# Kernel tuning notes

Measured on AMD Instinct MI355X. Metric: run time of the kernel, lower is better.

The kernel has to match this reference:

```python
import jax, jax.numpy as jnp
import numpy as np

N_LEVELS = 16
N_FEATS = 2
TABLE_SIZE = 1 << 19          # log2_hashmap_size = 19
BASE_RES = 32
PER_LEVEL_SCALE = 1.3819
RES = 512
CLAMP = 25.133
PRIME_Y = np.uint32(2654435761)
N_PTS = 1 << 19


def hashgrid_encode(table, uv):
    """Instant-NGP style multires hashgrid. table: [L, T, F], uv: [N, 2] in [0,1].
    Returns [N, L*F]."""
    L, T, F = table.shape
    levels = jnp.arange(L)
    res = jnp.floor(BASE_RES * (PER_LEVEL_SCALE ** levels.astype(jnp.float32))).astype(jnp.int32)  # [L]
    # 4 bilinear corner offsets
    offs = jnp.array([[0, 0], [1, 0], [0, 1], [1, 1]], dtype=jnp.int32)  # [4, 2]

    def level_fn(tab_l, res_l):
        pos = uv * res_l.astype(uv.dtype)                       # [N, 2]
        p0 = jnp.clip(jnp.floor(pos).astype(jnp.int32), 0, res_l - 1)
        frac = pos - p0.astype(uv.dtype)                        # [N, 2]
        corners = p0[:, None, :] + offs[None, :, :]             # [N, 4, 2]
        cx = corners[..., 0].astype(jnp.uint32)
        cy = corners[..., 1].astype(jnp.uint32)
        stride = (res_l + 1).astype(jnp.uint32)
        dense_idx = cx + cy * stride                            # dense grid index
        hash_idx = (cx ^ (cy * PRIME_Y)) & jnp.uint32(T - 1)    # spatial hash (T is pow2)
        use_dense = (res_l + 1).astype(jnp.int64) * (res_l + 1).astype(jnp.int64) <= T
        idx = jnp.where(use_dense, dense_idx, hash_idx).astype(jnp.int32)  # [N, 4]
        feats = tab_l[idx]                                      # [N, 4, F] gather
        wx, wy = frac[:, 0], frac[:, 1]
        w = jnp.stack([(1 - wx) * (1 - wy), wx * (1 - wy),
                       (1 - wx) * wy, wx * wy], axis=-1)        # [N, 4]
        return jnp.einsum('ncf,nc->nf', feats, w)               # [N, F]

    out = jax.vmap(level_fn)(table, res)                        # [L, N, F]
    return out.transpose(1, 0, 2).reshape(uv.shape[0], L * F)


def sin_layer(x, W, b):
    h = jnp.clip(x @ W.T + b, -CLAMP, CLAMP)
    return jnp.sin(h)


def setup_inputs() -> dict:
    key = jax.random.key(0)
    ks = jax.random.split(key, 8)
    y = jax.random.randint(ks[0], (N_PTS,), 0, RES, dtype=jnp.int32)
    x = jax.random.randint(ks[1], (N_PTS,), 0, RES, dtype=jnp.int32)
    cam_feat = jax.random.normal(ks[2], (32,), dtype=jnp.float32)
    # NGP tables initialized uniform in [-1e-4, 1e-4]
    table = jax.random.uniform(ks[3], (N_LEVELS, TABLE_SIZE, N_FEATS),
                               minval=-1e-4, maxval=1e-4, dtype=jnp.float32)
    def siren_w(k, outp, inp):
        return jax.random.uniform(k, (outp, inp), minval=-1.0 / inp, maxval=1.0 / inp,
                                  dtype=jnp.float32)
    W1 = siren_w(ks[4], 512, 64)
    W2 = siren_w(ks[5], 512, 512)
    W3 = siren_w(ks[6], 384, 512)
    return {"y": y, "x": x, "cam_feat": cam_feat, "table": table,
            "W1": W1, "b1": jnp.zeros((512,), jnp.float32),
            "W2": W2, "b2": jnp.zeros((512,), jnp.float32),
            "W3": W3, "b3": jnp.zeros((384,), jnp.float32)}


def reference(y, x, cam_feat, table, W1, b1, W2, b2, W3, b3):
    denom = jnp.float32(RES - 1)
    uv = jnp.stack([jnp.clip(x.astype(jnp.float32), 0, RES - 1) / denom,
                    jnp.clip(y.astype(jnp.float32), 0, RES - 1) / denom], axis=-1)  # [N, 2]
    codes = hashgrid_encode(table, uv)                          # [N, 32]
    cam = jnp.broadcast_to(cam_feat[None, :], (codes.shape[0], cam_feat.shape[0]))
    h = jnp.concatenate([codes, cam], axis=-1)                  # [N, 64]
    h = sin_layer(h, W1, b1)
    h = sin_layer(h, W2, b2)
    return sin_layer(h, W3, b3)                                 # [N, 384]
```

## Files before the change

### kernel.cpp

```cpp
#include <hip/hip_runtime.h>

typedef _Float16 half8 __attribute__((ext_vector_type(8)));
typedef _Float16 half4 __attribute__((ext_vector_type(4)));
typedef _Float16 half2v __attribute__((ext_vector_type(2)));
typedef float f32x4 __attribute__((ext_vector_type(4)));

#define TSIZE (1 << 19)
#define TMASK (TSIZE - 1)

__constant__ int c_res[16] = {32, 44, 61, 84, 116, 161, 222, 307,
                              425, 588, 812, 1123, 1551, 2144, 2963, 4095};

__global__ void hg_cvt_all(const float* __restrict__ W1, const float* __restrict__ W2,
                           const float* __restrict__ W3, _Float16* __restrict__ d) {
  int g = blockIdx.x * blockDim.x + threadIdx.x;
  int i = g * 4;
  const float* s;
  if (i < 32768) s = W1 + i;
  else if (i < 32768 + 262144) s = W2 + (i - 32768);
  else s = W3 + (i - 32768 - 262144);
  float4 v = *(const float4*)s;
  half4 h = {(_Float16)v.x, (_Float16)v.y, (_Float16)v.z, (_Float16)v.w};
  *(half4*)(d + i) = h;
}

__device__ __forceinline__ float sin_act_precise(float x) {
  if (__builtin_expect(fabsf(x) > 1.0f, 0))
    return sinf(fminf(fmaxf(x, -25.133f), 25.133f));
  float x2 = x * x;
  float p = 2.75573192e-6f;
  p = fmaf(p, x2, -1.98412698e-4f);
  p = fmaf(p, x2, 8.33333333e-3f);
  p = fmaf(p, x2, -1.66666667e-1f);
  return fmaf(p * x2, x, x);
}

__device__ __forceinline__ float sin_act_fast(float x) {
  return __sinf(fminf(fmaxf(x, -25.133f), 25.133f));
}

#define XROW 144
#define SBASE 18432
#define SROW 1040
#define LD_X(m, k) (*(const half8*)(&smem[(m) * XROW + (k) * 2]))
#define LD_S(m, k) (*(const half8*)(&smem[SBASE + (m) * SROW + (k) * 2]))
#define ST_S8(m, n, v) \
  do { *(half4*)(&smem[SBASE + (m) * SROW + (n) * 2]) = (v); } while (0)

#define MFMA16 __builtin_amdgcn_mfma_f32_16x16x32_f16

__global__ void __launch_bounds__(1024, 4)
hg_fused(const int* __restrict__ ybuf, const int* __restrict__ xbuf,
         const float* __restrict__ cam, const float* __restrict__ table,
         const _Float16* __restrict__ W1h, const float* __restrict__ b1,
         const _Float16* __restrict__ W2h, const float* __restrict__ b2,
         const _Float16* __restrict__ W3h, const float* __restrict__ b3,
         float* __restrict__ out) {
  __shared__ __align__(16) unsigned char smem[151552];
  const int t = threadIdx.x;
  const int lane = t & 63;
  const int wid = t >> 6;
  const int l15 = lane & 15;
  const int lhi = lane >> 4;
  const int rowh = wid & 1;
  const int colg = wid >> 1;
  const int mrow0 = rowh * 64;
  const int pbase = blockIdx.x << 7;
  const f32x4 vzero = {0.f, 0.f, 0.f, 0.f};

  {
    const int sub = t & 15;
    const int res = c_res[sub];
    const float rf = (float)res;
    const unsigned strd = (unsigned)(res + 1);
    const bool dense = (res <= 723);
    const float* tb = table + ((size_t)sub * TSIZE) * 2;
    const float2 cf = ((const float2*)cam)[sub];
    const half2v hc = {(_Float16)cf.x, (_Float16)cf.y};
#pragma unroll
    for (int hh = 0; hh < 2; ++hh) {
      const int m = (t >> 4) + hh * 64;
      const int p = pbase + m;
      const float u = (float)xbuf[p] / 511.0f;
      const float v = (float)ybuf[p] / 511.0f;
      const float px = u * rf, py = v * rf;
      int p0x = (int)floorf(px); p0x = p0x < 0 ? 0 : (p0x > res - 1 ? res - 1 : p0x);
      int p0y = (int)floorf(py); p0y = p0y < 0 ? 0 : (p0y > res - 1 ? res - 1 : p0y);
      const float fx = px - (float)p0x, fy = py - (float)p0y;
      const float w00 = (1.f - fx) * (1.f - fy), w10 = fx * (1.f - fy);
      const float w01 = (1.f - fx) * fy, w11 = fx * fy;
      float c0 = 0.f, c1 = 0.f;
#pragma unroll
      for (int c = 0; c < 4; ++c) {
        const unsigned cx = (unsigned)(p0x + (c & 1));
        const unsigned cy = (unsigned)(p0y + (c >> 1));
        const unsigned idx = dense ? (cx + cy * strd)
                                   : ((cx ^ (cy * 2654435761u)) & TMASK);
        const float2 f = *(const float2*)(tb + (size_t)idx * 2);
        const float w = (c == 0) ? w00 : (c == 1) ? w10 : (c == 2) ? w01 : w11;
        c0 = fmaf(w, f.x, c0);
        c1 = fmaf(w, f.y, c1);
      }
      half2v hf = {(_Float16)c0, (_Float16)c1};
      *(half2v*)(&smem[m * XROW + 4 * sub]) = hf;
      *(half2v*)(&smem[m * XROW + 64 + 4 * sub]) = hc;
    }
  }
  __syncthreads();

  {
    const int n0 = colg << 6;
    f32x4 acc[4][4];
#pragma unroll
    for (int i = 0; i < 4; ++i)
#pragma unroll
      for (int j = 0; j < 4; ++j) acc[i][j] = vzero;
#pragma unroll
    for (int ks = 0; ks < 2; ++ks) {
      const int kk = ks * 32 + lhi * 8;
      half8 bw[4];
#pragma unroll
      for (int nf = 0; nf < 4; ++nf)
        bw[nf] = *(const half8*)(W1h + (n0 + nf * 16 + l15) * 64 + kk);
      half8 ax[4];
#pragma unroll
      for (int mf = 0; mf < 4; ++mf) ax[mf] = LD_X(mrow0 + mf * 16 + l15, kk);
#pragma unroll
      for (int mf = 0; mf < 4; ++mf)
#pragma unroll
        for (int nf = 0; nf < 4; ++nf)
          acc[mf][nf] = MFMA16(bw[nf], ax[mf], acc[mf][nf], 0, 0, 0);
    }
#pragma unroll
    for (int nf = 0; nf < 4; ++nf) {
      const int nb = n0 + nf * 16 + lhi * 4;
      const f32x4 bb = *(const f32x4*)(b1 + nb);
#pragma unroll
      for (int mf = 0; mf < 4; ++mf) {
        half4 pk;
#pragma unroll
        for (int r = 0; r < 4; ++r)
          pk[r] = (_Float16)sin_act_fast(acc[mf][nf][r] + bb[r]);
        ST_S8(mrow0 + mf * 16 + l15, nb, pk);
      }
    }
  }
  __syncthreads();

  {
    const int n0 = colg << 6;
    f32x4 acc[4][4];
#pragma unroll
    for (int i = 0; i < 4; ++i)
#pragma unroll
      for (int j = 0; j < 4; ++j) acc[i][j] = vzero;
    half8 bw[4];
#pragma unroll
    for (int nf = 0; nf < 4; ++nf)
      bw[nf] = *(const half8*)(W2h + (n0 + nf * 16 + l15) * 512 + lhi * 8);
#pragma unroll 2
    for (int ks = 0; ks < 16; ++ks) {
      const int kkn = ((ks + 1) & 15) * 32 + lhi * 8;
      half8 nbw[4];
#pragma unroll
      for (int nf = 0; nf < 4; ++nf)
        nbw[nf] = *(const half8*)(W2h + (n0 + nf * 16 + l15) * 512 + kkn);
      const int kk = ks * 32 + lhi * 8;
      half8 ax[4];
#pragma unroll
      for (int mf = 0; mf < 4; ++mf) ax[mf] = LD_S(mrow0 + mf * 16 + l15, kk);
#pragma unroll
      for (int mf = 0; mf < 4; ++mf)
#pragma unroll
        for (int nf = 0; nf < 4; ++nf)
          acc[mf][nf] = MFMA16(bw[nf], ax[mf], acc[mf][nf], 0, 0, 0);
#pragma unroll
      for (int nf = 0; nf < 4; ++nf) bw[nf] = nbw[nf];
    }
    __syncthreads();
#pragma unroll
    for (int nf = 0; nf < 4; ++nf) {
      const int nb = n0 + nf * 16 + lhi * 4;
      const f32x4 bb = *(const f32x4*)(b2 + nb);
#pragma unroll
      for (int mf = 0; mf < 4; ++mf) {
        half4 pk;
#pragma unroll
        for (int r = 0; r < 4; ++r)
          pk[r] = (_Float16)sin_act_fast(acc[mf][nf][r] + bb[r]);
        ST_S8(mrow0 + mf * 16 + l15, nb, pk);
      }
    }
  }
  __syncthreads();

  {
    const int n0 = colg * 48;
    f32x4 acc[4][3];
#pragma unroll
    for (int i = 0; i < 4; ++i)
#pragma unroll
      for (int j = 0; j < 3; ++j) acc[i][j] = vzero;
    half8 bw[3];
#pragma unroll
    for (int nf = 0; nf < 3; ++nf)
      bw[nf] = *(const half8*)(W3h + (n0 + nf * 16 + l15) * 512 + lhi * 8);
#pragma unroll 2
    for (int ks = 0; ks < 16; ++ks) {
      const int kkn = ((ks + 1) & 15) * 32 + lhi * 8;
      half8 nbw[3];
#pragma unroll
      for (int nf = 0; nf < 3; ++nf)
        nbw[nf] = *(const half8*)(W3h + (n0 + nf * 16 + l15) * 512 + kkn);
      const int kk = ks * 32 + lhi * 8;
      half8 ax[4];
#pragma unroll
      for (int mf = 0; mf < 4; ++mf) ax[mf] = LD_S(mrow0 + mf * 16 + l15, kk);
#pragma unroll
      for (int mf = 0; mf < 4; ++mf)
#pragma unroll
        for (int nf = 0; nf < 3; ++nf)
          acc[mf][nf] = MFMA16(bw[nf], ax[mf], acc[mf][nf], 0, 0, 0);
#pragma unroll
      for (int nf = 0; nf < 3; ++nf) bw[nf] = nbw[nf];
    }
#pragma unroll
    for (int nf = 0; nf < 3; ++nf) {
      const int nb = n0 + nf * 16 + lhi * 4;
      const f32x4 bb = *(const f32x4*)(b3 + nb);
#pragma unroll
      for (int mf = 0; mf < 4; ++mf) {
        float4 o;
        float* op = &o.x;
#pragma unroll
        for (int r = 0; r < 4; ++r)
          op[r] = sin_act_precise(acc[mf][nf][r] + bb[r]);
        *(float4*)(out + (size_t)(pbase + mrow0 + mf * 16 + l15) * 384 + nb) = o;
      }
    }
  }
}

extern "C" void kernel_launch(void* const* d_in, const int* in_sizes, int n_in,
                              void* d_out, int out_size, void* d_ws, size_t ws_size,
                              hipStream_t stream) {
  const int* y = (const int*)d_in[0];
  const int* x = (const int*)d_in[1];
  const float* cam = (const float*)d_in[2];
  const float* table = (const float*)d_in[3];
  const float* W1 = (const float*)d_in[4];
  const float* b1 = (const float*)d_in[5];
  const float* W2 = (const float*)d_in[6];
  const float* b2 = (const float*)d_in[7];
  const float* W3 = (const float*)d_in[8];
  const float* b3 = (const float*)d_in[9];
  float* out = (float*)d_out;

  _Float16* Wh = (_Float16*)d_ws;
  _Float16* W1h = Wh;
  _Float16* W2h = W1h + 512 * 64;
  _Float16* W3h = W2h + 512 * 512;

  hg_cvt_all<<<480, 256, 0, stream>>>(W1, W2, W3, Wh);

  const int nblocks = (1 << 19) / 128;
  hg_fused<<<nblocks, 1024, 0, stream>>>(y, x, cam, table, W1h, b1, W2h, b2, W3h, b3, out);
}
```

Measured before the change: 1.322 ms.

## Split fused MLP kernel into three per-layer kernels staging activations in output buffer

Splits the single fused kernel (hashgrid encode plus three SIREN layers) into three kernels: encode+layer1, layer2, and layer3. Intermediate fp16 activations are staged through global memory in the output buffer, which each later kernel overwrites in place. The layer 2 and 3 kernels use 512 threads with 8 M-fragments per wave and a smaller shared-memory footprint, aiming for better occupancy and weight reuse. The cost is extra global round-trips for the 512-wide activations and two extra launches; the in-place reuse also depends on each block touching only its own rows.

Result: slower. 1.430 ms (+8.1%).

```diff
diff --git a/kernel.cpp b/kernel.cpp
--- a/kernel.cpp
+++ b/kernel.cpp
@@ -7,6 +7,7 @@
 
 #define TSIZE (1 << 19)
 #define TMASK (TSIZE - 1)
+#define SLOT 1536
 
 __constant__ int c_res[16] = {32, 44, 61, 84, 116, 161, 222, 307,
                               425, 588, 812, 1123, 1551, 2144, 2963, 4095};
@@ -36,27 +37,19 @@
 }
 
 __device__ __forceinline__ float sin_act_fast(float x) {
-  return __sinf(fminf(fmaxf(x, -25.133f), 25.133f));
-}
-
+  return __sinf(__builtin_amdgcn_fmed3f(x, -25.133f, 25.133f));
+}
+
+#define MFMA16 __builtin_amdgcn_mfma_f32_16x16x32_f16
 #define XROW 144
-#define SBASE 18432
 #define SROW 1040
-#define LD_X(m, k) (*(const half8*)(&smem[(m) * XROW + (k) * 2]))
-#define LD_S(m, k) (*(const half8*)(&smem[SBASE + (m) * SROW + (k) * 2]))
-#define ST_S8(m, n, v) \
-  do { *(half4*)(&smem[SBASE + (m) * SROW + (n) * 2]) = (v); } while (0)
-
-#define MFMA16 __builtin_amdgcn_mfma_f32_16x16x32_f16
 
 __global__ void __launch_bounds__(1024, 4)
-hg_fused(const int* __restrict__ ybuf, const int* __restrict__ xbuf,
-         const float* __restrict__ cam, const float* __restrict__ table,
-         const _Float16* __restrict__ W1h, const float* __restrict__ b1,
-         const _Float16* __restrict__ W2h, const float* __restrict__ b2,
-         const _Float16* __restrict__ W3h, const float* __restrict__ b3,
-         float* __restrict__ out) {
-  __shared__ __align__(16) unsigned char smem[151552];
+hg_encode_l1(const int* __restrict__ ybuf, const int* __restrict__ xbuf,
+             const float* __restrict__ cam, const float* __restrict__ table,
+             const _Float16* __restrict__ W1h, const float* __restrict__ b1,
+             char* __restrict__ outb) {
+  __shared__ __align__(16) unsigned char smem[128 * XROW];
   const int t = threadIdx.x;
   const int lane = t & 63;
   const int wid = t >> 6;
@@ -124,7 +117,8 @@
         bw[nf] = *(const half8*)(W1h + (n0 + nf * 16 + l15) * 64 + kk);
       half8 ax[4];
 #pragma unroll
-      for (int mf = 0; mf < 4; ++mf) ax[mf] = LD_X(mrow0 + mf * 16 + l15, kk);
+      for (int mf = 0; mf < 4; ++mf)
+        ax[mf] = *(const half8*)(&smem[(mrow0 + mf * 16 + l15) * XROW + kk * 2]);
 #pragma unroll
       for (int mf = 0; mf < 4; ++mf)
 #pragma unroll
@@ -141,102 +135,125 @@
 #pragma unroll
         for (int r = 0; r < 4; ++r)
           pk[r] = (_Float16)sin_act_fast(acc[mf][nf][r] + bb[r]);
-        ST_S8(mrow0 + mf * 16 + l15, nb, pk);
+        *(half4*)(outb + (size_t)(pbase + mrow0 + mf * 16 + l15) * SLOT + nb * 2) = pk;
       }
     }
   }
+}
+
+__global__ void __launch_bounds__(512, 2)
+hg_l2(const _Float16* __restrict__ W2h, const float* __restrict__ b2,
+      char* __restrict__ outb) {
+  __shared__ __align__(16) unsigned char smem[128 * SROW];
+  const int t = threadIdx.x;
+  const int lane = t & 63;
+  const int wid = t >> 6;
+  const int l15 = lane & 15;
+  const int lhi = lane >> 4;
+  const int pbase = blockIdx.x << 7;
+  const f32x4 vzero = {0.f, 0.f, 0.f, 0.f};
+
+#pragma unroll
+  for (int i = 0; i < 16; ++i) {
+    const int idx = i * 512 + t;
+    const int p = idx >> 6;
+    const int seg = idx & 63;
+    const half8 v = *(const half8*)(outb + (size_t)(pbase + p) * SLOT + seg * 16);
+    *(half8*)(&smem[p * SROW + seg * 16]) = v;
+  }
   __syncthreads();
 
-  {
-    const int n0 = colg << 6;
-    f32x4 acc[4][4];
-#pragma unroll
-    for (int i = 0; i < 4; ++i)
-#pragma unroll
-      for (int j = 0; j < 4; ++j) acc[i][j] = vzero;
+  const int n0 = wid << 6;
+  f32x4 acc[8][4];
+#pragma unroll
+  for (int i = 0; i < 8; ++i)
+#pragma unroll
+    for (int j = 0; j < 4; ++j) acc[i][j] = vzero;
+#pragma unroll 2
+  for (int ks = 0; ks < 16; ++ks) {
+    const int kk = ks * 32 + lhi * 8;
     half8 bw[4];
 #pragma unroll
     for (int nf = 0; nf < 4; ++nf)
-      bw[nf] = *(const half8*)(W2h + (n0 + nf * 16 + l15) * 512 + lhi * 8);
+      bw[nf] = *(const half8*)(W2h + (n0 + nf * 16 + l15) * 512 + kk);
+#pragma unroll
+    for (int mf = 0; mf < 8; ++mf) {
+      const half8 ax = *(const half8*)(&smem[(mf * 16 + l15) * SROW + kk * 2]);
+#pragma unroll
+      for (int nf = 0; nf < 4; ++nf)
+        acc[mf][nf] = MFMA16(bw[nf], ax, acc[mf][nf], 0, 0, 0);
+    }
+  }
+#pragma unroll
+  for (int nf = 0; nf < 4; ++nf) {
+    const int nb = n0 + nf * 16 + lhi * 4;
+    const f32x4 bb = *(const f32x4*)(b2 + nb);
+#pragma unroll
+    for (int mf = 0; mf < 8; ++mf) {
+      half4 pk;
+#pragma unroll
+      for (int r = 0; r < 4; ++r)
+        pk[r] = (_Float16)sin_act_fast(acc[mf][nf][r] + bb[r]);
+      *(half4*)(outb + (size_t)(pbase + mf * 16 + l15) * SLOT + nb * 2) = pk;
+    }
+  }
+}
+
+__global__ void __launch_bounds__(512, 2)
+hg_l3(const _Float16* __restrict__ W3h, const float* __restrict__ b3,
+      char* __restrict__ outb) {
+  __shared__ __align__(16) unsigned char smem[128 * SROW];
+  const int t = threadIdx.x;
+  const int lane = t & 63;
+  const int wid = t >> 6;
+  const int l15 = lane & 15;
+  const int lhi = lane >> 4;
+  const int pbase = blockIdx.x << 7;
+  const f32x4 vzero = {0.f, 0.f, 0.f, 0.f};
+
+#pragma unroll
+  for (int i = 0; i < 16; ++i) {
+    const int idx = i * 512 + t;
+    const int p = idx >> 6;
+    const int seg = idx & 63;
+    const half8 v = *(const half8*)(outb + (size_t)(pbase + p) * SLOT + seg * 16);
+    *(half8*)(&smem[p * SROW + seg * 16]) = v;
+  }
+  __syncthreads();
+
+  const int n0 = wid * 48;
+  f32x4 acc[8][3];
+#pragma unroll
+  for (int i = 0; i < 8; ++i)
+#pragma unroll
+    for (int j = 0; j < 3; ++j) acc[i][j] = vzero;
 #pragma unroll 2
-    for (int ks = 0; ks < 16; ++ks) {
-      const int kkn = ((ks + 1) & 15) * 32 + lhi * 8;
-      half8 nbw[4];
-#pragma unroll
-      for (int nf = 0; nf < 4; ++nf)
-        nbw[nf] = *(const half8*)(W2h + (n0 + nf * 16 + l15) * 512 + kkn);
-      const int kk = ks * 32 + lhi * 8;
-      half8 ax[4];
-#pragma unroll
-      for (int mf = 0; mf < 4; ++mf) ax[mf] = LD_S(mrow0 + mf * 16 + l15, kk);
-#pragma unroll
-      for (int mf = 0; mf < 4; ++mf)
-#pragma unroll
-        for (int nf = 0; nf < 4; ++nf)
-          acc[mf][nf] = MFMA16(bw[nf], ax[mf], acc[mf][nf], 0, 0, 0);
-#pragma unroll
-      for (int nf = 0; nf < 4; ++nf) bw[nf] = nbw[nf];
-    }
-    __syncthreads();
-#pragma unroll
-    for (int nf = 0; nf < 4; ++nf) {
-      const int nb = n0 + nf * 16 + lhi * 4;
-      const f32x4 bb = *(const f32x4*)(b2 + nb);
-#pragma unroll
-      for (int mf = 0; mf < 4; ++mf) {
-        half4 pk;
-#pragma unroll
-        for (int r = 0; r < 4; ++r)
-          pk[r] = (_Float16)sin_act_fast(acc[mf][nf][r] + bb[r]);
-        ST_S8(mrow0 + mf * 16 + l15, nb, pk);
-      }
-    }
-  }
-  __syncthreads();
-
-  {
-    const int n0 = colg * 48;
-    f32x4 acc[4][3];
-#pragma unroll
-    for (int i = 0; i < 4; ++i)
-#pragma unroll
-      for (int j = 0; j < 3; ++j) acc[i][j] = vzero;
+  for (int ks = 0; ks < 16; ++ks) {
+    const int kk = ks * 32 + lhi * 8;
     half8 bw[3];
 #pragma unroll
     for (int nf = 0; nf < 3; ++nf)
-      bw[nf] = *(const half8*)(W3h + (n0 + nf * 16 + l15) * 512 + lhi * 8);
-#pragma unroll 2
-    for (int ks = 0; ks < 16; ++ks) {
-      const int kkn = ((ks + 1) & 15) * 32 + lhi * 8;
-      half8 nbw[3];
+      bw[nf] = *(const half8*)(W3h + (n0 + nf * 16 + l15) * 512 + kk);
+#pragma unroll
+    for (int mf = 0; mf < 8; ++mf) {
+      const half8 ax = *(const half8*)(&smem[(mf * 16 + l15) * SROW + kk * 2]);
 #pragma unroll
       for (int nf = 0; nf < 3; ++nf)
-        nbw[nf] = *(const half8*)(W3h + (n0 + nf * 16 + l15) * 512 + kkn);
-      const int kk = ks * 32 + lhi * 8;
-      half8 ax[4];
-#pragma unroll
-      for (int mf = 0; mf < 4; ++mf) ax[mf] = LD_S(mrow0 + mf * 16 + l15, kk);
-#pragma unroll
-      for (int mf = 0; mf < 4; ++mf)
-#pragma unroll
-        for (int nf = 0; nf < 3; ++nf)
-          acc[mf][nf] = MFMA16(bw[nf], ax[mf], acc[mf][nf], 0, 0, 0);
-#pragma unroll
-      for (int nf = 0; nf < 3; ++nf) bw[nf] = nbw[nf];
-    }
-#pragma unroll
-    for (int nf = 0; nf < 3; ++nf) {
-      const int nb = n0 + nf * 16 + lhi * 4;
-      const f32x4 bb = *(const f32x4*)(b3 + nb);
-#pragma unroll
-      for (int mf = 0; mf < 4; ++mf) {
-        float4 o;
-        float* op = &o.x;
-#pragma unroll
-        for (int r = 0; r < 4; ++r)
-          op[r] = sin_act_precise(acc[mf][nf][r] + bb[r]);
-        *(float4*)(out + (size_t)(pbase + mrow0 + mf * 16 + l15) * 384 + nb) = o;
-      }
+        acc[mf][nf] = MFMA16(bw[nf], ax, acc[mf][nf], 0, 0, 0);
+    }
+  }
+#pragma unroll
+  for (int nf = 0; nf < 3; ++nf) {
+    const int nb = n0 + nf * 16 + lhi * 4;
+    const f32x4 bb = *(const f32x4*)(b3 + nb);
+#pragma unroll
+    for (int mf = 0; mf < 8; ++mf) {
+      float4 o;
+      float* op = &o.x;
+#pragma unroll
+      for (int r = 0; r < 4; ++r)
+        op[r] = sin_act_precise(acc[mf][nf][r] + bb[r]);
+      *(float4*)(outb + (size_t)(pbase + mf * 16 + l15) * SLOT + nb * 4) = o;
     }
   }
 }
@@ -254,7 +271,7 @@
   const float* b2 = (const float*)d_in[7];
   const float* W3 = (const float*)d_in[8];
   const float* b3 = (const float*)d_in[9];
-  float* out = (float*)d_out;
+  char* outb = (char*)d_out;
 
   _Float16* Wh = (_Float16*)d_ws;
   _Float16* W1h = Wh;
@@ -264,5 +281,7 @@
   hg_cvt_all<<<480, 256, 0, stream>>>(W1, W2, W3, Wh);
 
   const int nblocks = (1 << 19) / 128;
-  hg_fused<<<nblocks, 1024, 0, stream>>>(y, x, cam, table, W1h, b1, W2h, b2, W3h, b3, out);
-}
+  hg_encode_l1<<<nblocks, 1024, 0, stream>>>(y, x, cam, table, W1h, b1, outb);
+  hg_l2<<<nblocks, 512, 0, stream>>>(W2h, b2, outb);
+  hg_l3<<<nblocks, 512, 0, stream>>>(W3h, b3, outb);
+}
```
